# Optimization experiments

Measured on AMD Instinct MI355X. Metric: run time of the kernel, lower is better.

## Reference

```python
import jax, jax.numpy as jnp
import numpy as np

B, T, H, F = 32, 2048, 1024, 1024  # batch, kv_len, hidden_size, feature_size


def setup_inputs() -> dict:
    key = jax.random.key(0)
    ks = jax.random.split(key, 6)
    s = 0.02  # param init scale
    return {
        "query": jax.random.normal(ks[0], (B, 1, H), jnp.float32),
        "keys": jax.random.normal(ks[1], (B, T, F), jnp.float32),
        "Wa_w": jax.random.normal(ks[2], (H, H), jnp.float32) * s,
        "Wa_b": jnp.zeros((H,), jnp.float32),
        "Ua_w": jax.random.normal(ks[3], (H, F), jnp.float32) * s,
        "Ua_b": jnp.zeros((H,), jnp.float32),
        "Va_w": jax.random.normal(ks[4], (1, H), jnp.float32) * s,
        "Va_b": jnp.zeros((1,), jnp.float32),
    }


def reference(query, keys, Wa_w, Wa_b, Ua_w, Ua_b, Va_w, Va_b):
    # Wa(query): [B,1,H]; Ua(keys): [B,T,H]
    q = jnp.einsum('bqh,oh->bqo', query, Wa_w) + Wa_b
    k = jnp.einsum('btf,of->bto', keys, Ua_w) + Ua_b
    e = jnp.tanh(q + k)                                   # [B,T,H] (broadcast over q dim of size 1)
    scores = jnp.einsum('bth,h->bt', e, Va_w[0]) + Va_b[0]  # Va(...).squeeze(2) -> [B,T]
    scores = scores[:, None, :]                           # unsqueeze(1) -> [B,1,T]
    weights = jax.nn.softmax(scores, axis=-1)             # [B,1,T]
    context = jnp.einsum('bqt,btf->bqf', weights, keys)   # bmm -> [B,1,F]
    return context, weights
```

## Files before the change

kernel.cpp:

```cpp
#include <hip/hip_runtime.h>
#include <hip/hip_bf16.h>

typedef float  f32x4 __attribute__((ext_vector_type(4)));
typedef short  s16x8 __attribute__((ext_vector_type(8)));
typedef __hip_bfloat16 bf16;

#define BDIM 32
#define TDIM 2048
#define HDIM 1024
#define FDIM 1024
#define MTOT (BDIM*TDIM)

#define GLOAD16(gp, lp) __builtin_amdgcn_global_load_lds(                     \
    (const __attribute__((address_space(1))) void*)(gp),                      \
    (__attribute__((address_space(3))) void*)(lp), 16, 0, 0)

#define MFMA_BF16 __builtin_amdgcn_mfma_f32_16x16x32_bf16

__global__ __launch_bounds__(256) void cvt_bf16_kernel(
    const float* __restrict__ src, bf16* __restrict__ dst, int n8)
{
    int i = blockIdx.x * 256 + threadIdx.x;
    const int stride = gridDim.x * 256;
    for (; i < n8; i += stride) {
        const f32x4 a = ((const f32x4*)src)[2 * i];
        const f32x4 b = ((const f32x4*)src)[2 * i + 1];
        union { bf16 h[8]; s16x8 v; } u;
        #pragma unroll
        for (int j = 0; j < 4; ++j) {
            u.h[j]     = __float2bfloat16(a[j]);
            u.h[4 + j] = __float2bfloat16(b[j]);
        }
        ((s16x8*)dst)[i] = u.v;
    }
}

__global__ __launch_bounds__(256) void qeff_kernel(
    const float* __restrict__ query, const float* __restrict__ Wa_w,
    const float* __restrict__ Wa_b,  const float* __restrict__ Ua_b,
    float* __restrict__ qe)
{
    const int lane = threadIdx.x & 63;
    const int gw   = blockIdx.x * 4 + (threadIdx.x >> 6);
    const int b    = gw >> 10;
    const int o    = gw & 1023;
    const float* qp = query + (size_t)b * HDIM;
    const float* wp = Wa_w  + (size_t)o * HDIM;
    float s = 0.f;
    #pragma unroll
    for (int i = 0; i < 16; ++i) {
        const int h = i * 64 + lane;
        s += qp[h] * wp[h];
    }
    #pragma unroll
    for (int off = 32; off > 0; off >>= 1) s += __shfl_down(s, off);
    if (lane == 0) qe[gw] = s + Wa_b[o] + Ua_b[o];
}

#define STAGE_A(buf_, kb_, h_, s_) GLOAD16(                                    \
    Ab + (size_t)(M0 + (h_)*128 + (((s_)>>1)<<4) + srow) * FDIM               \
       + (kb_) + (((s_)&1)<<5) + scg*8,                                        \
    &As[buf_][((((h_)*8 + ((s_)>>1)) * 2 + ((s_)&1)) << 9)])
#define STAGE_B(buf_, n0_, kb_, h_, s_) GLOAD16(                               \
    Bb + (size_t)((n0_) + (h_)*128 + (((s_)>>1)<<4) + srow) * FDIM            \
       + (kb_) + (((s_)&1)<<5) + scg*8,                                        \
    &Bs[buf_][((((h_)*8 + ((s_)>>1)) * 2 + ((s_)&1)) << 9)])

__global__ __launch_bounds__(512) void score_gemm_256_kernel(
    const bf16* __restrict__ Ab, const bf16* __restrict__ Bb,
    const float* __restrict__ qe, const float* __restrict__ Va,
    float* __restrict__ part_out)
{
    __shared__ bf16 As[2][16384];
    __shared__ bf16 Bs[2][16384];
    __shared__ float red[4][256];

    const int tid  = threadIdx.x;
    const int lane = tid & 63;
    const int w    = tid >> 6;
    const int wr   = w >> 2;
    const int wc   = w & 3;

    const int bid = blockIdx.x;
    const int mt  = (bid & 7) * 32 + (bid >> 3);
    const int M0  = mt * 256;

    const int srow = lane >> 2;
    const int scg  = (lane & 3) ^ (((lane >> 5) & 1) << 1);
    const int r    = lane & 15;
    const int q4   = lane >> 4;
    const int roff = r * 32 + ((q4 ^ (((r >> 3) & 1) << 1)) & 3) * 8;

    const int bb = M0 >> 11;
    const float* qrow = qe + (size_t)bb * HDIM;

    STAGE_B(0, 0, 0, 0, w); STAGE_B(0, 0, 0, 0, w + 8);
    STAGE_B(0, 0, 0, 1, w); STAGE_B(0, 0, 0, 1, w + 8);
    STAGE_A(0, 0, 0, w); STAGE_A(0, 0, 0, w + 8);
    STAGE_A(0, 0, 1, w); STAGE_A(0, 0, 1, w + 8);
    STAGE_B(1, 0, 64, 0, w); STAGE_B(1, 0, 64, 0, w + 8);
    STAGE_B(1, 0, 64, 1, w); STAGE_B(1, 0, 64, 1, w + 8);

    for (int g = 0; g < 4; ++g) {
        const int N0 = g << 8;

        asm volatile("s_waitcnt vmcnt(4)" ::: "memory");
        __builtin_amdgcn_s_barrier();
        __builtin_amdgcn_sched_barrier(0);

        f32x4 acc[8][4];
        #pragma unroll
        for (int m = 0; m < 8; ++m)
            #pragma unroll
            for (int n = 0; n < 4; ++n) acc[m][n] = (f32x4){0.f, 0.f, 0.f, 0.f};

        for (int i = 0; i < 8; ++i) {
            const bool pf  = (i < 7);
            const int kbO1 = (2 * i + 1) << 6;
            const int kbE2 = (2 * i + 2) << 6;
            const int kbO2 = (2 * i + 3) << 6;

            s16x8 a0[4][2], a1[4][2], b0[2][2], b1[2][2];

            #pragma unroll
            for (int mf = 0; mf < 4; ++mf)
                #pragma unroll
                for (int ks = 0; ks < 2; ++ks)
                    a0[mf][ks] = *(const s16x8*)
                        &As[0][(((wr * 8 + mf) * 2 + ks) << 9) + roff];
            #pragma unroll
            for (int nf = 0; nf < 2; ++nf)
                #pragma unroll
                for (int ks = 0; ks < 2; ++ks)
                    b0[nf][ks] = *(const s16x8*)
                        &Bs[0][(((wc * 4 + nf) * 2 + ks) << 9) + roff];
            STAGE_A(1, kbO1, 0, w); STAGE_A(1, kbO1, 0, w + 8);
            __builtin_amdgcn_s_setprio(1);
            #pragma unroll
            for (int mf = 0; mf < 4; ++mf)
                #pragma unroll
                for (int nf = 0; nf < 2; ++nf)
                    #pragma unroll
                    for (int ks = 0; ks < 2; ++ks)
                        acc[mf][nf] = MFMA_BF16(a0[mf][ks], b0[nf][ks],
                                                acc[mf][nf], 0, 0, 0);
            __builtin_amdgcn_s_setprio(0);
            __builtin_amdgcn_s_barrier();

            #pragma unroll
            for (int nf = 0; nf < 2; ++nf)
                #pragma unroll
                for (int ks = 0; ks < 2; ++ks)
                    b1[nf][ks] = *(const s16x8*)
                        &Bs[0][(((wc * 4 + 2 + nf) * 2 + ks) << 9) + roff];
            STAGE_A(1, kbO1, 1, w); STAGE_A(1, kbO1, 1, w + 8);
            __builtin_amdgcn_s_setprio(1);
            #pragma unroll
            for (int mf = 0; mf < 4; ++mf)
                #pragma unroll
                for (int nf = 0; nf < 2; ++nf)
                    #pragma unroll
                    for (int ks = 0; ks < 2; ++ks)
                        acc[mf][2 + nf] = MFMA_BF16(a0[mf][ks], b1[nf][ks],
                                                    acc[mf][2 + nf], 0, 0, 0);
            __builtin_amdgcn_s_setprio(0);
            __builtin_amdgcn_s_barrier();

            #pragma unroll
            for (int mf = 0; mf < 4; ++mf)
                #pragma unroll
                for (int ks = 0; ks < 2; ++ks)
                    a1[mf][ks] = *(const s16x8*)
                        &As[0][(((wr * 8 + 4 + mf) * 2 + ks) << 9) + roff];
            if (pf) { STAGE_B(0, N0, kbE2, 0, w); STAGE_B(0, N0, kbE2, 0, w + 8); }
            __builtin_amdgcn_s_setprio(1);
            #pragma unroll
            for (int mf = 0; mf < 4; ++mf)
                #pragma unroll
                for (int nf = 0; nf < 2; ++nf)
                    #pragma unroll
                    for (int ks = 0; ks < 2; ++ks)
                        acc[4 + mf][nf] = MFMA_BF16(a1[mf][ks], b0[nf][ks],
                                                    acc[4 + mf][nf], 0, 0, 0);
            __builtin_amdgcn_s_setprio(0);
            __builtin_amdgcn_s_barrier();

            if (pf) { STAGE_B(0, N0, kbE2, 1, w); STAGE_B(0, N0, kbE2, 1, w + 8); }
            __builtin_amdgcn_s_setprio(1);
            #pragma unroll
            for (int mf = 0; mf < 4; ++mf)
                #pragma unroll
                for (int nf = 0; nf < 2; ++nf)
                    #pragma unroll
                    for (int ks = 0; ks < 2; ++ks)
                        acc[4 + mf][2 + nf] = MFMA_BF16(a1[mf][ks], b1[nf][ks],
                                                        acc[4 + mf][2 + nf], 0, 0, 0);
            __builtin_amdgcn_s_setprio(0);
            if (pf) asm volatile("s_waitcnt vmcnt(4)" ::: "memory");
            else    asm volatile("s_waitcnt vmcnt(0)" ::: "memory");
            __builtin_amdgcn_s_barrier();
            __builtin_amdgcn_sched_barrier(0);

            #pragma unroll
            for (int mf = 0; mf < 4; ++mf)
                #pragma unroll
                for (int ks = 0; ks < 2; ++ks)
                    a0[mf][ks] = *(const s16x8*)
                        &As[1][(((wr * 8 + mf) * 2 + ks) << 9) + roff];
            #pragma unroll
            for (int nf = 0; nf < 2; ++nf)
                #pragma unroll
                for (int ks = 0; ks < 2; ++ks)
                    b0[nf][ks] = *(const s16x8*)
                        &Bs[1][(((wc * 4 + nf) * 2 + ks) << 9) + roff];
            if (pf) { STAGE_A(0, kbE2, 0, w); STAGE_A(0, kbE2, 0, w + 8); }
            __builtin_amdgcn_s_setprio(1);
            #pragma unroll
            for (int mf = 0; mf < 4; ++mf)
                #pragma unroll
                for (int nf = 0; nf < 2; ++nf)
                    #pragma unroll
                    for (int ks = 0; ks < 2; ++ks)
                        acc[mf][nf] = MFMA_BF16(a0[mf][ks], b0[nf][ks],
                                                acc[mf][nf], 0, 0, 0);
            __builtin_amdgcn_s_setprio(0);
            __builtin_amdgcn_s_barrier();

            #pragma unroll
            for (int nf = 0; nf < 2; ++nf)
                #pragma unroll
                for (int ks = 0; ks < 2; ++ks)
                    b1[nf][ks] = *(const s16x8*)
                        &Bs[1][(((wc * 4 + 2 + nf) * 2 + ks) << 9) + roff];
            if (pf) { STAGE_A(0, kbE2, 1, w); STAGE_A(0, kbE2, 1, w + 8); }
            __builtin_amdgcn_s_setprio(1);
            #pragma unroll
            for (int mf = 0; mf < 4; ++mf)
                #pragma unroll
                for (int nf = 0; nf < 2; ++nf)
                    #pragma unroll
                    for (int ks = 0; ks < 2; ++ks)
                        acc[mf][2 + nf] = MFMA_BF16(a0[mf][ks], b1[nf][ks],
                                                    acc[mf][2 + nf], 0, 0, 0);
            __builtin_amdgcn_s_setprio(0);
            __builtin_amdgcn_s_barrier();

            #pragma unroll
            for (int mf = 0; mf < 4; ++mf)
                #pragma unroll
                for (int ks = 0; ks < 2; ++ks)
                    a1[mf][ks] = *(const s16x8*)
                        &As[1][(((wr * 8 + 4 + mf) * 2 + ks) << 9) + roff];
            if (pf) { STAGE_B(1, N0, kbO2, 0, w); STAGE_B(1, N0, kbO2, 0, w + 8); }
            __builtin_amdgcn_s_setprio(1);
            #pragma unroll
            for (int mf = 0; mf < 4; ++mf)
                #pragma unroll
                for (int nf = 0; nf < 2; ++nf)
                    #pragma unroll
                    for (int ks = 0; ks < 2; ++ks)
                        acc[4 + mf][nf] = MFMA_BF16(a1[mf][ks], b0[nf][ks],
                                                    acc[4 + mf][nf], 0, 0, 0);
            __builtin_amdgcn_s_setprio(0);
            __builtin_amdgcn_s_barrier();

            if (pf) { STAGE_B(1, N0, kbO2, 1, w); STAGE_B(1, N0, kbO2, 1, w + 8); }
            __builtin_amdgcn_s_setprio(1);
            #pragma unroll
            for (int mf = 0; mf < 4; ++mf)
                #pragma unroll
                for (int nf = 0; nf < 2; ++nf)
                    #pragma unroll
                    for (int ks = 0; ks < 2; ++ks)
                        acc[4 + mf][2 + nf] = MFMA_BF16(a1[mf][ks], b1[nf][ks],
                                                        acc[4 + mf][2 + nf], 0, 0, 0);
            __builtin_amdgcn_s_setprio(0);
            if (pf) {
                asm volatile("s_waitcnt vmcnt(4)" ::: "memory");
                __builtin_amdgcn_s_barrier();
                __builtin_amdgcn_sched_barrier(0);
            }
        }

        __builtin_amdgcn_s_barrier();

        if (g < 3) {
            const int n0n = (g + 1) << 8;
            STAGE_B(0, n0n, 0, 0, w); STAGE_B(0, n0n, 0, 0, w + 8);
            STAGE_B(0, n0n, 0, 1, w); STAGE_B(0, n0n, 0, 1, w + 8);
            STAGE_A(0, 0, 0, w); STAGE_A(0, 0, 0, w + 8);
            STAGE_A(0, 0, 1, w); STAGE_A(0, 0, 1, w + 8);
            STAGE_B(1, n0n, 64, 0, w); STAGE_B(1, n0n, 64, 0, w + 8);
            STAGE_B(1, n0n, 64, 1, w); STAGE_B(1, n0n, 64, 1, w + 8);
        }

        #pragma unroll
        for (int mf = 0; mf < 8; ++mf) {
            float part[4] = {0.f, 0.f, 0.f, 0.f};
            #pragma unroll
            for (int nf = 0; nf < 4; ++nf) {
                const int c    = N0 + wc * 64 + nf * 16 + (lane & 15);
                const float va = Va[c];
                const float qv = qrow[c];
                #pragma unroll
                for (int j = 0; j < 4; ++j) {
                    const float x = qv + acc[mf][nf][j];
                    const float e = __expf(2.0f * x);
                    part[j] += va * (1.0f - 2.0f / (e + 1.0f));
                }
            }
            #pragma unroll
            for (int j = 0; j < 4; ++j)
                #pragma unroll
                for (int off = 1; off < 16; off <<= 1)
                    part[j] += __shfl_xor(part[j], off);
            if ((lane & 15) == 0) {
                const int row = wr * 128 + mf * 16 + q4 * 4;
                float4 pv = {part[0], part[1], part[2], part[3]};
                *(float4*)&red[wc][row] = pv;
            }
        }
        asm volatile("s_waitcnt lgkmcnt(0)" ::: "memory");
        __builtin_amdgcn_s_barrier();

        if (tid < 256) {
            const float s4 = (red[0][tid] + red[1][tid])
                           + (red[2][tid] + red[3][tid]);
            part_out[(size_t)g * MTOT + M0 + tid] = s4;
        }
    }
}

__global__ __launch_bounds__(256) void score_gemm_f32_kernel(
    const float* __restrict__ keys, const float* __restrict__ Ua,
    const float* __restrict__ qe,   const float* __restrict__ Va,
    float* __restrict__ scores)
{
    __shared__ bf16 Asf[128][40];
    __shared__ bf16 Bsf[128][40];

    const int tid  = threadIdx.x;
    const int lane = tid & 63;
    const int wid  = tid >> 6;
    const int wr   = wid >> 1, wc = wid & 1;
    const int n0   = blockIdx.x * 128;
    const int m0   = blockIdx.y * 128;

    const int srow  = tid >> 1;
    const int shalf = tid & 1;
    const float* gA = keys + (size_t)(m0 + srow) * FDIM + shalf * 16;
    const float* gB = Ua   + (size_t)(n0 + srow) * FDIM + shalf * 16;

    f32x4 acc[4][4];
    #pragma unroll
    for (int m = 0; m < 4; ++m)
        #pragma unroll
        for (int n = 0; n < 4; ++n) acc[m][n] = (f32x4){0.f, 0.f, 0.f, 0.f};

    float4 ra[4], rbv[4];
    #pragma unroll
    for (int i = 0; i < 4; ++i) {
        ra[i]  = ((const float4*)gA)[i];
        rbv[i] = ((const float4*)gB)[i];
    }

    for (int kt = 0; kt < 32; ++kt) {
        __syncthreads();
        {
            union { bf16 h[16]; s16x8 v[2]; } ua, ub;
            #pragma unroll
            for (int i = 0; i < 4; ++i) {
                const float* fa = (const float*)&ra[i];
                const float* fb = (const float*)&rbv[i];
                #pragma unroll
                for (int j = 0; j < 4; ++j) {
                    ua.h[i*4+j] = __float2bfloat16(fa[j]);
                    ub.h[i*4+j] = __float2bfloat16(fb[j]);
                }
            }
            *(s16x8*)&Asf[srow][shalf*16]     = ua.v[0];
            *(s16x8*)&Asf[srow][shalf*16 + 8] = ua.v[1];
            *(s16x8*)&Bsf[srow][shalf*16]     = ub.v[0];
            *(s16x8*)&Bsf[srow][shalf*16 + 8] = ub.v[1];
        }
        __syncthreads();

        if (kt + 1 < 32) {
            const float* pa = gA + (kt + 1) * 32;
            const float* pb = gB + (kt + 1) * 32;
            #pragma unroll
            for (int i = 0; i < 4; ++i) {
                ra[i]  = ((const float4*)pa)[i];
                rbv[i] = ((const float4*)pb)[i];
            }
        }

        s16x8 af[4], bfr[4];
        #pragma unroll
        for (int m = 0; m < 4; ++m)
            af[m] = *(const s16x8*)&Asf[wr*64 + m*16 + (lane & 15)][(lane >> 4) * 8];
        #pragma unroll
        for (int n = 0; n < 4; ++n)
            bfr[n] = *(const s16x8*)&Bsf[wc*64 + n*16 + (lane & 15)][(lane >> 4) * 8];
        #pragma unroll
        for (int m = 0; m < 4; ++m)
            #pragma unroll
            for (int n = 0; n < 4; ++n)
                acc[m][n] = MFMA_BF16(af[m], bfr[n], acc[m][n], 0, 0, 0);
    }

    const int b = m0 >> 11;
    const float* qrow = qe + (size_t)b * HDIM;
    #pragma unroll
    for (int m = 0; m < 4; ++m) {
        float part[4] = {0.f, 0.f, 0.f, 0.f};
        #pragma unroll
        for (int n = 0; n < 4; ++n) {
            const int c    = n0 + wc*64 + n*16 + (lane & 15);
            const float va = Va[c];
            const float qv = qrow[c];
            #pragma unroll
            for (int j = 0; j < 4; ++j) {
                const float x = qv + acc[m][n][j];
                const float e = __expf(2.0f * x);
                part[j] += va * (1.0f - 2.0f / (e + 1.0f));
            }
        }
        #pragma unroll
        for (int j = 0; j < 4; ++j)
            #pragma unroll
            for (int off = 1; off < 16; off <<= 1)
                part[j] += __shfl_xor(part[j], off);
        if ((lane & 15) == 0) {
            const int rr = m0 + wr*64 + m*16 + (lane >> 4) * 4;
            #pragma unroll
            for (int j = 0; j < 4; ++j) atomicAdd(&scores[rr + j], part[j]);
        }
    }
}

__global__ __launch_bounds__(256) void softmax_partial_kernel(
    const float* __restrict__ part, float* __restrict__ sw)
{
    const int b    = blockIdx.x;
    const int tid  = threadIdx.x;
    const int lane = tid & 63, wid = tid >> 6;
    __shared__ float red[8];

    float v[8];
    float m = -3.4e38f;
    #pragma unroll
    for (int i = 0; i < 8; ++i) {
        const size_t idx = (size_t)b * TDIM + i * 256 + tid;
        v[i] = (part[idx] + part[idx + MTOT])
             + (part[idx + 2 * (size_t)MTOT] + part[idx + 3 * (size_t)MTOT]);
        m = fmaxf(m, v[i]);
    }
    #pragma unroll
    for (int off = 32; off > 0; off >>= 1) m = fmaxf(m, __shfl_xor(m, off));
    if (lane == 0) red[wid] = m;
    __syncthreads();
    m = fmaxf(fmaxf(red[0], red[1]), fmaxf(red[2], red[3]));

    float s = 0.f;
    #pragma unroll
    for (int i = 0; i < 8; ++i) { v[i] = __expf(v[i] - m); s += v[i]; }
    #pragma unroll
    for (int off = 32; off > 0; off >>= 1) s += __shfl_xor(s, off);
    if (lane == 0) red[4 + wid] = s;
    __syncthreads();
    s = (red[4] + red[5]) + (red[6] + red[7]);

    const float inv = 1.0f / s;
    #pragma unroll
    for (int i = 0; i < 8; ++i) sw[b * TDIM + i * 256 + tid] = v[i] * inv;
}

__global__ __launch_bounds__(256) void softmax_kernel(float* __restrict__ sw)
{
    const int b    = blockIdx.x;
    const int tid  = threadIdx.x;
    const int lane = tid & 63, wid = tid >> 6;
    __shared__ float red[8];

    float v[8];
    float m = -3.4e38f;
    #pragma unroll
    for (int i = 0; i < 8; ++i) {
        v[i] = sw[b * TDIM + i * 256 + tid];
        m = fmaxf(m, v[i]);
    }
    #pragma unroll
    for (int off = 32; off > 0; off >>= 1) m = fmaxf(m, __shfl_xor(m, off));
    if (lane == 0) red[wid] = m;
    __syncthreads();
    m = fmaxf(fmaxf(red[0], red[1]), fmaxf(red[2], red[3]));

    float s = 0.f;
    #pragma unroll
    for (int i = 0; i < 8; ++i) { v[i] = __expf(v[i] - m); s += v[i]; }
    #pragma unroll
    for (int off = 32; off > 0; off >>= 1) s += __shfl_xor(s, off);
    if (lane == 0) red[4 + wid] = s;
    __syncthreads();
    s = (red[4] + red[5]) + (red[6] + red[7]);

    const float inv = 1.0f / s;
    #pragma unroll
    for (int i = 0; i < 8; ++i) sw[b * TDIM + i * 256 + tid] = v[i] * inv;
}

__global__ __launch_bounds__(256) void context_bf16_kernel(
    const bf16* __restrict__ keys, const float* __restrict__ w,
    float* __restrict__ ctx)
{
    const int tc  = blockIdx.x;
    const int b   = blockIdx.y;
    const int tid = threadIdx.x;
    __shared__ float ws_[128];
    if (tid < 128) ws_[tid] = w[b * TDIM + tc * 128 + tid];
    __syncthreads();

    const bf16* kp = keys + ((size_t)b * TDIM + (size_t)tc * 128) * FDIM + tid * 4;
    float4 acc = {0.f, 0.f, 0.f, 0.f};
    #pragma unroll 8
    for (int t = 0; t < 128; ++t) {
        const short4 kv = *(const short4*)(kp + (size_t)t * FDIM);
        const float wt = ws_[t];
        acc.x += wt * __uint_as_float(((unsigned)(unsigned short)kv.x) << 16);
        acc.y += wt * __uint_as_float(((unsigned)(unsigned short)kv.y) << 16);
        acc.z += wt * __uint_as_float(((unsigned)(unsigned short)kv.z) << 16);
        acc.w += wt * __uint_as_float(((unsigned)(unsigned short)kv.w) << 16);
    }
    float* cp = ctx + (size_t)b * FDIM + tid * 4;
    atomicAdd(cp + 0, acc.x); atomicAdd(cp + 1, acc.y);
    atomicAdd(cp + 2, acc.z); atomicAdd(cp + 3, acc.w);
}

__global__ __launch_bounds__(256) void context_f32_kernel(
    const float* __restrict__ keys, const float* __restrict__ w,
    float* __restrict__ ctx)
{
    const int tc  = blockIdx.x;
    const int b   = blockIdx.y;
    const int tid = threadIdx.x;
    __shared__ float ws_[128];
    if (tid < 128) ws_[tid] = w[b * TDIM + tc * 128 + tid];
    __syncthreads();

    const float* kp = keys + ((size_t)b * TDIM + (size_t)tc * 128) * FDIM + tid * 4;
    float4 acc = {0.f, 0.f, 0.f, 0.f};
    #pragma unroll 8
    for (int t = 0; t < 128; ++t) {
        const float4 kv = *(const float4*)(kp + (size_t)t * FDIM);
        const float wt = ws_[t];
        acc.x += wt * kv.x; acc.y += wt * kv.y;
        acc.z += wt * kv.z; acc.w += wt * kv.w;
    }
    float* cp = ctx + (size_t)b * FDIM + tid * 4;
    atomicAdd(cp + 0, acc.x); atomicAdd(cp + 1, acc.y);
    atomicAdd(cp + 2, acc.z); atomicAdd(cp + 3, acc.w);
}

extern "C" void kernel_launch(void* const* d_in, const int* in_sizes, int n_in,
                              void* d_out, int out_size, void* d_ws, size_t ws_size,
                              hipStream_t stream)
{
    const float* query = (const float*)d_in[0];
    const float* keys  = (const float*)d_in[1];
    const float* Wa_w  = (const float*)d_in[2];
    const float* Wa_b  = (const float*)d_in[3];
    const float* Ua_w  = (const float*)d_in[4];
    const float* Ua_b  = (const float*)d_in[5];
    const float* Va_w  = (const float*)d_in[6];

    float* out = (float*)d_out;
    float* ctx = out;
    float* sw  = out + BDIM * HDIM;

    const size_t needA = (size_t)MTOT * FDIM * sizeof(bf16);
    const size_t needB = (size_t)HDIM * FDIM * sizeof(bf16);
    const size_t needP = (size_t)4 * MTOT * sizeof(float);
    const bool fast = ws_size >= needA + needB + needP;

    qeff_kernel<<<dim3(BDIM * HDIM / 4), 256, 0, stream>>>(query, Wa_w, Wa_b, Ua_b, ctx);

    if (fast) {
        bf16*  Ab      = (bf16*)d_ws;
        bf16*  Bb      = Ab + (size_t)MTOT * FDIM;
        float* partial = (float*)(Bb + (size_t)HDIM * FDIM);
        cvt_bf16_kernel<<<dim3(2048), 256, 0, stream>>>(keys, Ab, MTOT * FDIM / 8);
        cvt_bf16_kernel<<<dim3(512),  256, 0, stream>>>(Ua_w, Bb, HDIM * FDIM / 8);
        score_gemm_256_kernel<<<dim3(256), 512, 0, stream>>>(Ab, Bb, ctx, Va_w, partial);
        softmax_partial_kernel<<<dim3(BDIM), 256, 0, stream>>>(partial, sw);
        hipMemsetAsync(ctx, 0, (size_t)BDIM * HDIM * sizeof(float), stream);
        context_bf16_kernel<<<dim3(16, BDIM), 256, 0, stream>>>(Ab, sw, ctx);
    } else {
        hipMemsetAsync(sw, 0, (size_t)BDIM * TDIM * sizeof(float), stream);
        score_gemm_f32_kernel<<<dim3(HDIM / 128, MTOT / 128), 256, 0, stream>>>(
            keys, Ua_w, ctx, Va_w, sw);
        softmax_kernel<<<dim3(BDIM), 256, 0, stream>>>(sw);
        hipMemsetAsync(ctx, 0, (size_t)BDIM * HDIM * sizeof(float), stream);
        context_f32_kernel<<<dim3(16, BDIM), 256, 0, stream>>>(keys, sw, ctx);
    }
}
```

Measured before the change: 271.7 us.

## Restructure context kernel to split features across blocks and drop atomics

The context reduction now gives each block a 128-wide feature slice across the full sequence, rather than a 128-row time chunk. Partial sums are reduced in shared memory and written with plain stores, which removes the memset and the global atomicAdds. The launch shrinks from 512 to 256 blocks, and each thread's 8-byte loads now cover only a 256-byte row segment per warp, so parallelism and coalescing may suffer on this memory-bound step.

```diff
diff --git a/kernel.cpp b/kernel.cpp
--- a/kernel.cpp
+++ b/kernel.cpp
@@ -16,6 +16,7 @@
     (__attribute__((address_space(3))) void*)(lp), 16, 0, 0)
 
 #define MFMA_BF16 __builtin_amdgcn_mfma_f32_16x16x32_bf16
+#define BF2F(x) __uint_as_float(((unsigned)(unsigned short)(x)) << 16)
 
 __global__ __launch_bounds__(256) void cvt_bf16_kernel(
     const float* __restrict__ src, bf16* __restrict__ dst, int n8)
@@ -510,31 +511,46 @@
     for (int i = 0; i < 8; ++i) sw[b * TDIM + i * 256 + tid] = v[i] * inv;
 }
 
-__global__ __launch_bounds__(256) void context_bf16_kernel(
+__global__ __launch_bounds__(256) void context_nb_kernel(
     const bf16* __restrict__ keys, const float* __restrict__ w,
     float* __restrict__ ctx)
 {
-    const int tc  = blockIdx.x;
+    const int fc  = blockIdx.x;
     const int b   = blockIdx.y;
     const int tid = threadIdx.x;
-    __shared__ float ws_[128];
-    if (tid < 128) ws_[tid] = w[b * TDIM + tc * 128 + tid];
+    const int c   = tid & 31;
+    const int rg  = tid >> 5;
+
+    __shared__ float wsh[TDIM];
+    __shared__ float4 red4[8][32];
+
+    #pragma unroll
+    for (int i = 0; i < 8; ++i) wsh[i * 256 + tid] = w[b * TDIM + i * 256 + tid];
     __syncthreads();
 
-    const bf16* kp = keys + ((size_t)b * TDIM + (size_t)tc * 128) * FDIM + tid * 4;
+    const bf16* kp = keys + ((size_t)b * TDIM + rg) * FDIM + fc * 128 + c * 4;
     float4 acc = {0.f, 0.f, 0.f, 0.f};
-    #pragma unroll 8
-    for (int t = 0; t < 128; ++t) {
-        const short4 kv = *(const short4*)(kp + (size_t)t * FDIM);
-        const float wt = ws_[t];
-        acc.x += wt * __uint_as_float(((unsigned)(unsigned short)kv.x) << 16);
-        acc.y += wt * __uint_as_float(((unsigned)(unsigned short)kv.y) << 16);
-        acc.z += wt * __uint_as_float(((unsigned)(unsigned short)kv.z) << 16);
-        acc.w += wt * __uint_as_float(((unsigned)(unsigned short)kv.w) << 16);
-    }
-    float* cp = ctx + (size_t)b * FDIM + tid * 4;
-    atomicAdd(cp + 0, acc.x); atomicAdd(cp + 1, acc.y);
-    atomicAdd(cp + 2, acc.z); atomicAdd(cp + 3, acc.w);
+    #pragma unroll 4
+    for (int t = rg; t < TDIM; t += 8) {
+        const short4 kv = *(const short4*)(kp + (size_t)(t - rg) * FDIM);
+        const float wt = wsh[t];
+        acc.x += wt * BF2F(kv.x);
+        acc.y += wt * BF2F(kv.y);
+        acc.z += wt * BF2F(kv.z);
+        acc.w += wt * BF2F(kv.w);
+    }
+    red4[rg][c] = acc;
+    __syncthreads();
+
+    if (rg == 0) {
+        float4 s = red4[0][c];
+        #pragma unroll
+        for (int k = 1; k < 8; ++k) {
+            const float4 p = red4[k][c];
+            s.x += p.x; s.y += p.y; s.z += p.z; s.w += p.w;
+        }
+        *(float4*)&ctx[(size_t)b * FDIM + fc * 128 + c * 4] = s;
+    }
 }
 
 __global__ __launch_bounds__(256) void context_f32_kernel(
@@ -593,8 +609,7 @@
         cvt_bf16_kernel<<<dim3(512),  256, 0, stream>>>(Ua_w, Bb, HDIM * FDIM / 8);
         score_gemm_256_kernel<<<dim3(256), 512, 0, stream>>>(Ab, Bb, ctx, Va_w, partial);
         softmax_partial_kernel<<<dim3(BDIM), 256, 0, stream>>>(partial, sw);
-        hipMemsetAsync(ctx, 0, (size_t)BDIM * HDIM * sizeof(float), stream);
-        context_bf16_kernel<<<dim3(16, BDIM), 256, 0, stream>>>(Ab, sw, ctx);
+        context_nb_kernel<<<dim3(8, BDIM), 256, 0, stream>>>(Ab, sw, ctx);
     } else {
         hipMemsetAsync(sw, 0, (size_t)BDIM * TDIM * sizeof(float), stream);
         score_gemm_f32_kernel<<<dim3(HDIM / 128, MTOT / 128), 256, 0, stream>>>(
```

After: 273.4 us. No clear change (+0.6%).
